# Optimization experiments

Hardware: AMD Instinct MI355X
Metric: run time of the kernel (lower is better)

The kernel has to match this reference:

```python
import jax, jax.numpy as jnp
import numpy as np

EPS = 1e-5
DIM, QK, PDIM = 448, 16, 96

def _bn(y, w, b, rm, rv):
    # inference-mode BatchNorm2d over channel axis 1
    scale = (w / jnp.sqrt(rv + EPS))[None, :, None, None]
    return (y - rm[None, :, None, None]) * scale + b[None, :, None, None]

def setup_inputs() -> dict:
    key = jax.random.key(0)
    ks = jax.random.split(key, 13)
    B, H, W = 64, 32, 32
    return {
        "x": jax.random.normal(ks[0], (B, DIM, H, W), jnp.float32),
        "gn_w": jax.random.uniform(ks[1], (PDIM,), jnp.float32, 0.5, 1.5),
        "gn_b": 0.02 * jax.random.normal(ks[2], (PDIM,), jnp.float32),
        "qkv_w": jax.random.normal(ks[3], (2 * QK + PDIM, PDIM), jnp.float32) * (PDIM ** -0.5),
        "qkv_bn_w": jax.random.uniform(ks[4], (2 * QK + PDIM,), jnp.float32, 0.5, 1.5),
        "qkv_bn_b": 0.02 * jax.random.normal(ks[5], (2 * QK + PDIM,), jnp.float32),
        "qkv_bn_rm": 0.02 * jax.random.normal(ks[6], (2 * QK + PDIM,), jnp.float32),
        "qkv_bn_rv": jax.random.uniform(ks[7], (2 * QK + PDIM,), jnp.float32, 0.5, 1.5),
        "proj_w": jax.random.normal(ks[8], (DIM, DIM), jnp.float32) * (DIM ** -0.5),
        "proj_bn_w": jax.random.uniform(ks[9], (DIM,), jnp.float32, 0.5, 1.5),
        "proj_bn_b": 0.02 * jax.random.normal(ks[10], (DIM,), jnp.float32),
        "proj_bn_rm": 0.02 * jax.random.normal(ks[11], (DIM,), jnp.float32),
        "proj_bn_rv": jax.random.uniform(ks[12], (DIM,), jnp.float32, 0.5, 1.5),
    }

def reference(x, gn_w, gn_b, qkv_w, qkv_bn_w, qkv_bn_b, qkv_bn_rm, qkv_bn_rv,
              proj_w, proj_bn_w, proj_bn_b, proj_bn_rm, proj_bn_rv):
    B, C, H, W = x.shape
    scale = QK ** -0.5
    x1, x2 = x[:, :PDIM], x[:, PDIM:]
    # GroupNorm with num_groups=1: normalize over (C,H,W) per sample
    mu = jnp.mean(x1, axis=(1, 2, 3), keepdims=True)
    var = jnp.var(x1, axis=(1, 2, 3), keepdims=True)
    x1n = (x1 - mu) * jax.lax.rsqrt(var + EPS)
    x1n = x1n * gn_w[None, :, None, None] + gn_b[None, :, None, None]
    # 1x1 conv (no bias) + BN
    qkv = jnp.einsum('bchw,oc->bohw', x1n, qkv_w)
    qkv = _bn(qkv, qkv_bn_w, qkv_bn_b, qkv_bn_rm, qkv_bn_rv)
    q, k, v = qkv[:, :QK], qkv[:, QK:2 * QK], qkv[:, 2 * QK:]
    N = H * W
    q = q.reshape(B, QK, N); k = k.reshape(B, QK, N); v = v.reshape(B, PDIM, N)
    attn = jnp.einsum('bcn,bcm->bnm', q, k) * scale          # [B,N,N]
    attn = jax.nn.softmax(attn, axis=-1)
    x1o = jnp.einsum('bcm,bnm->bcn', v, attn).reshape(B, PDIM, H, W)
    y = jnp.concatenate([x1o, x2], axis=1)
    y = jax.nn.relu(y)
    y = jnp.einsum('bchw,oc->bohw', y, proj_w)
    return _bn(y, proj_bn_w, proj_bn_b, proj_bn_rm, proj_bn_rv)
```

## Files before the change

### kernel.cpp

```cpp
#include <hip/hip_runtime.h>
#include <hip/hip_bf16.h>

#define EPS 1e-5f

constexpr int BB   = 64;
constexpr int CDIM = 448;
constexpr int PD   = 96;
constexpr int QKD  = 16;
constexpr int QO   = 128;
constexpr int NPix = 1024;
constexpr int NCH  = 14;

constexpr size_t WS_MU  = 0;
constexpr size_t WS_RS  = 64;
constexpr size_t WS_QSC = 128;
constexpr size_t WS_QBI = 256;
constexpr size_t WS_PSC = 384;
constexpr size_t WS_PBI = 832;
constexpr size_t WS_WG  = 1280;
constexpr size_t WS_SWG = 13568;
constexpr size_t WS_WB  = 13696;
constexpr size_t WS_WGT = 13824;
constexpr size_t WS_WGH = 26112;
constexpr size_t WS_YB  = 32768;
constexpr size_t WS_W16 = WS_YB + (size_t)BB*NPix*CDIM/2;
constexpr size_t WS_QT  = WS_W16 + (size_t)512*CDIM/2;
constexpr size_t WS_KT  = WS_QT + (size_t)BB*NPix*32/2;
constexpr size_t WS_VB  = WS_KT + (size_t)BB*NPix*32/2;

typedef __attribute__((ext_vector_type(8))) short short8;
typedef __attribute__((ext_vector_type(8))) _Float16 half8;
typedef __attribute__((ext_vector_type(4))) float f32x4;

__device__ __forceinline__ unsigned short f2bf(float v) {
  __hip_bfloat16 h = __float2bfloat16(v);
  return *reinterpret_cast<unsigned short*>(&h);
}
__device__ __forceinline__ unsigned short f2h(float v) {
  _Float16 h = (_Float16)v;
  return *reinterpret_cast<unsigned short*>(&h);
}

typedef const __attribute__((address_space(1))) unsigned int* gp_t;
typedef __attribute__((address_space(3))) unsigned int* lp_t;
__device__ __forceinline__ void gload16(const void* g, void* l) {
  __builtin_amdgcn_global_load_lds((gp_t)g, (lp_t)l, 16, 0, 0);
}

constexpr int XT_BLOCKS = 11264;
constexpr int TAILB     = 209;
__global__ __launch_bounds__(256) void k_setup(
    const float* __restrict__ x,
    const float* __restrict__ gn_w, const float* __restrict__ gn_b,
    const float* __restrict__ qkv_w,
    const float* __restrict__ qbw, const float* __restrict__ qbb,
    const float* __restrict__ qbrm, const float* __restrict__ qbrv,
    const float* __restrict__ pw,
    const float* __restrict__ pbw, const float* __restrict__ pbb,
    const float* __restrict__ pbrm, const float* __restrict__ pbrv,
    float* __restrict__ ws, unsigned short* __restrict__ Wb,
    unsigned short* __restrict__ Ybc) {
  __shared__ float tile[32][65];
  float* red = &tile[0][0];
  int t = threadIdx.x;
  if (blockIdx.x >= TAILB) {
    int idx = blockIdx.x - TAILB;
    int nx = idx & 15, cy = (idx >> 4) % 11, b = idx / 176;
    int c0 = PD + cy * 32;
    int n0 = nx * 64;
#pragma unroll
    for (int i = 0; i < 2; ++i) {
      int k = t + i * 256;
      int c = k >> 4, q = k & 15;
      float4 v = reinterpret_cast<const float4*>(
                     x + ((size_t)b * CDIM + c0 + c) * NPix + n0)[q];
      *reinterpret_cast<float4*>(&tile[c][q * 4]) = v;
    }
    __syncthreads();
    int n = t >> 2, ch = t & 3;
    short8 o;
#pragma unroll
    for (int j = 0; j < 8; ++j)
      o[j] = (short)f2bf(fmaxf(tile[ch * 8 + j][n], 0.f));
    *reinterpret_cast<short8*>(
        &Ybc[(((size_t)b * NCH + 3 + cy) * NPix + n0 + n) * 32 + ch * 8]) = o;
    return;
  }
  int bid = blockIdx.x;
  if (bid < 64) {
    int b = bid;
    const float4* x4 = reinterpret_cast<const float4*>(x + (size_t)b * CDIM * NPix);
    float s = 0.f, ss = 0.f;
#pragma unroll 8
    for (int ii = 0; ii < PD * NPix / 4 / 256; ++ii) {
      float4 v = x4[t + ii * 256];
      s  += v.x + v.y + v.z + v.w;
      ss += v.x * v.x + v.y * v.y + v.z * v.z + v.w * v.w;
    }
#pragma unroll
    for (int o = 32; o > 0; o >>= 1) { s += __shfl_down(s, o); ss += __shfl_down(ss, o); }
    int wid = t >> 6;
    if ((t & 63) == 0) { red[wid] = s; red[4 + wid] = ss; }
    __syncthreads();
    if (t == 0) {
      float S  = red[0] + red[1] + red[2] + red[3];
      float SS = red[4] + red[5] + red[6] + red[7];
      const float inv_n = 1.f / (PD * NPix);
      float mu  = S * inv_n;
      float var = SS * inv_n - mu * mu;
      ws[WS_MU + b] = mu;
      ws[WS_RS + b] = rsqrtf(var + EPS);
    }
  } else if (bid < 96) {
    int o = (bid - 64) * 4 + (t >> 6);
    int lane = t & 63;
    unsigned short* Wgh = reinterpret_cast<unsigned short*>(ws + WS_WGH);
    float sw = 0.f, bb = 0.f;
    for (int c = lane; c < PD; c += 64) {
      float w  = qkv_w[o * PD + c];
      float wg = w * gn_w[c];
      Wgh[(size_t)o * PD + c] = f2h(wg);
      sw += wg;
      bb += w * gn_b[c];
    }
#pragma unroll
    for (int off = 32; off > 0; off >>= 1) {
      sw += __shfl_down(sw, off);
      bb += __shfl_down(bb, off);
    }
    if (lane == 0) {
      ws[WS_SWG + o] = sw;
      ws[WS_WB + o]  = bb;
      float sc = qbw[o] * rsqrtf(qbrv[o] + EPS);
      ws[WS_QSC + o] = sc;
      ws[WS_QBI + o] = qbb[o] - qbrm[o] * sc;
    }
  } else if (bid == 96) {
    for (int o = t; o < CDIM; o += 256) {
      float sc = pbw[o] * rsqrtf(pbrv[o] + EPS);
      ws[WS_PSC + o] = sc;
      ws[WS_PBI + o] = pbb[o] - pbrm[o] * sc;
    }
  } else {
    int idx = (bid - 97) * 256 + t;
    int row = idx / 56, sl = (idx % 56) * 8;
    short8 o = {};
    if (row < CDIM) {
      const float* src = pw + (size_t)row * CDIM + sl;
#pragma unroll
      for (int j = 0; j < 8; ++j) o[j] = (short)f2bf(src[j]);
    }
    *reinterpret_cast<short8*>(&Wb[(size_t)row * CDIM + sl]) = o;
  }
}

__global__ __launch_bounds__(256) void k_qkv2(const float* __restrict__ x,
                                              float* __restrict__ ws,
                                              unsigned short* __restrict__ qt,
                                              unsigned short* __restrict__ kt,
                                              unsigned short* __restrict__ vb) {
  __shared__ __align__(16) char smem[PD * 132 * 4];
  float*          xt = reinterpret_cast<float*>(smem);
  unsigned short* ld = reinterpret_cast<unsigned short*>(smem);

  int lin = blockIdx.x + 8 * blockIdx.y;
  int swz = (lin & 7) * 64 + (lin >> 3);
  int n0  = (swz & 7) * 128;
  int b   = swz >> 3;
  int t   = threadIdx.x;
  int lane = t & 63, w = t >> 6;
  int lo = lane & 15, hi = lane >> 4;

  const float4* xb4 = reinterpret_cast<const float4*>(x + (size_t)b * CDIM * NPix);
#pragma unroll
  for (int i = 0; i < 12; ++i) {
    int idx = t + i * 256;
    int row = idx >> 5, c4 = idx & 31;
    float4 v = xb4[row * (NPix / 4) + (n0 >> 2) + c4];
    *reinterpret_cast<float4*>(&xt[row * 132 + c4 * 4]) = v;
  }
  __syncthreads();

  const unsigned short* Wgh = reinterpret_cast<const unsigned short*>(ws + WS_WGH);
  f32x4 acc[8][2] = {{{}}};
#pragma unroll
  for (int kk = 0; kk < 3; ++kk) {
    half8 bfr[2];
#pragma unroll
    for (int nf = 0; nf < 2; ++nf) {
      int nr = w * 32 + nf * 16 + lo;
      half8 h;
#pragma unroll
      for (int j = 0; j < 8; ++j)
        h[j] = (_Float16)xt[(kk * 32 + hi * 8 + j) * 132 + nr];
      bfr[nf] = h;
    }
#pragma unroll
    for (int of = 0; of < 8; ++of) {
      half8 a = *reinterpret_cast<const half8*>(
          &Wgh[(size_t)(of * 16 + lo) * PD + kk * 32 + hi * 8]);
      acc[of][0] = __builtin_amdgcn_mfma_f32_16x16x32_f16(a, bfr[0], acc[of][0], 0, 0, 0);
      acc[of][1] = __builtin_amdgcn_mfma_f32_16x16x32_f16(a, bfr[1], acc[of][1], 0, 0, 0);
    }
  }
  float mu = ws[WS_MU + b], rs = ws[WS_RS + b];
  __syncthreads();
#pragma unroll
  for (int of = 0; of < 8; ++of) {
#pragma unroll
    for (int r = 0; r < 4; ++r) {
      int o = of * 16 + hi * 4 + r;
      float bias = ws[WS_WB + o] - rs * mu * ws[WS_SWG + o];
      float qs = ws[WS_QSC + o], qb = ws[WS_QBI + o];
      float postm = (o < QKD) ? 0.25f : 1.f;
#pragma unroll
      for (int nf = 0; nf < 2; ++nf) {
        int nl = w * 32 + nf * 16 + lo;
        float v = (qs * (rs * acc[of][nf][r] + bias) + qb) * postm;
        ld[o * 136 + nl] = f2h(v);
      }
    }
  }
  __syncthreads();
#pragma unroll
  for (int i = 0; i < 6; ++i) {
    int idx = t + i * 256;
    int row = idx >> 4, c8 = idx & 15;
    short8 v = *reinterpret_cast<const short8*>(&ld[(32 + row) * 136 + c8 * 8]);
    *reinterpret_cast<short8*>(&vb[((size_t)b * PD + row) * NPix + n0 + c8 * 8]) = v;
  }
#pragma unroll
  for (int i = 0; i < 4; ++i) {
    int idx = t + i * 256;
    int arr = idx >> 9;
    int rem = idx & 511;
    int n = rem >> 2, q4 = rem & 3;
    short8 o = {};
    if (q4 < 2) {
#pragma unroll
      for (int j = 0; j < 8; ++j)
        o[j] = (short)ld[(arr * 16 + q4 * 8 + j) * 136 + n];
    }
    unsigned short* dst = arr ? kt : qt;
    *reinterpret_cast<short8*>(&dst[((size_t)b * NPix + n0 + n) * 32 + q4 * 8]) = o;
  }
}

__global__ __launch_bounds__(512) void k_attn2(
    const unsigned short* __restrict__ qt,
    const unsigned short* __restrict__ kt,
    const unsigned short* __restrict__ vb,
    unsigned short* __restrict__ Ybc) {
  __shared__ __align__(16) unsigned short kt_s[128 * 40];
  __shared__ __align__(16) unsigned short vt_s[96 * 136];
  __shared__ __align__(16) unsigned short P_s[8 * 16 * 136];

  int lin = blockIdx.x + 8 * blockIdx.y;
  int swz = (lin & 7) * 64 + (lin >> 3);
  int n0  = (swz & 7) * 128;
  int b   = swz >> 3;
  int t  = threadIdx.x;
  int lane = t & 63, w = t >> 6;
  int lo = lane & 15, hi = lane >> 4;

  half8 q8 = *reinterpret_cast<const half8*>(
      &qt[((size_t)b * NPix + n0 + w * 16 + lo) * 32 + hi * 8]);

  const unsigned short* ktb = kt + (size_t)b * NPix * 32;
  const unsigned short* vbb = vb + (size_t)b * PD * NPix;

  f32x4 o[6] = {};
  float M = -1e30f, L = 0.f;
  f32x4 zero = {};

  for (int mt = 0; mt < 8; ++mt) {
    int m0 = mt * 128;
    int krow = t >> 2, kc4 = t & 3;
    float4 rk = *reinterpret_cast<const float4*>(&ktb[(size_t)(m0 + krow) * 32 + kc4 * 8]);
    float4 rv[3];
#pragma unroll
    for (int i = 0; i < 3; ++i) {
      int ci = t + 512 * i;
      int row = ci >> 4, c4 = ci & 15;
      rv[i] = *reinterpret_cast<const float4*>(&vbb[(size_t)row * NPix + m0 + c4 * 8]);
    }
    __syncthreads();
    *reinterpret_cast<float4*>(&kt_s[krow * 40 + kc4 * 8]) = rk;
#pragma unroll
    for (int i = 0; i < 3; ++i) {
      int ci = t + 512 * i;
      int row = ci >> 4, c4 = ci & 15;
      *reinterpret_cast<float4*>(&vt_s[row * 136 + c4 * 8]) = rv[i];
    }
    __syncthreads();

    f32x4 s[8];
    __builtin_amdgcn_s_setprio(1);
#pragma unroll
    for (int ss = 0; ss < 8; ++ss) {
      half8 a = *reinterpret_cast<const half8*>(&kt_s[(ss * 16 + lo) * 40 + hi * 8]);
      s[ss] = __builtin_amdgcn_mfma_f32_16x16x32_f16(a, q8, zero, 0, 0, 0);
    }
    __builtin_amdgcn_s_setprio(0);

    float tmax = s[0][0];
#pragma unroll
    for (int ss = 0; ss < 8; ++ss)
#pragma unroll
      for (int r = 0; r < 4; ++r) tmax = fmaxf(tmax, s[ss][r]);
    tmax = fmaxf(tmax, __shfl_xor(tmax, 16));
    tmax = fmaxf(tmax, __shfl_xor(tmax, 32));
    float newM = fmaxf(M, tmax);
    float fac = __expf(M - newM);
    M = newM;
    float psum = 0.f;
    unsigned pbase = (w * 16 + lo) * 136;
#pragma unroll
    for (int ss = 0; ss < 8; ++ss) {
      float p0 = __expf(s[ss][0] - M);
      float p1 = __expf(s[ss][1] - M);
      float p2 = __expf(s[ss][2] - M);
      float p3 = __expf(s[ss][3] - M);
      psum += (p0 + p1) + (p2 + p3);
      unsigned u01 = (unsigned)f2h(p0) | ((unsigned)f2h(p1) << 16);
      unsigned u23 = (unsigned)f2h(p2) | ((unsigned)f2h(p3) << 16);
      *reinterpret_cast<unsigned*>(&P_s[pbase + 16 * ss + 4 * hi])     = u01;
      *reinterpret_cast<unsigned*>(&P_s[pbase + 16 * ss + 4 * hi + 2]) = u23;
    }
    psum += __shfl_xor(psum, 16);
    psum += __shfl_xor(psum, 32);
    L = L * fac + psum;
#pragma unroll
    for (int cf = 0; cf < 6; ++cf)
#pragma unroll
      for (int r = 0; r < 4; ++r) o[cf][r] *= fac;
    asm volatile("s_waitcnt lgkmcnt(0)" ::: "memory");

    __builtin_amdgcn_s_setprio(1);
#pragma unroll
    for (int ks = 0; ks < 4; ++ks) {
      half8 pb = *reinterpret_cast<const half8*>(&P_s[pbase + ks * 32 + hi * 8]);
#pragma unroll
      for (int cf = 0; cf < 6; ++cf) {
        half8 va = *reinterpret_cast<const half8*>(&vt_s[(cf * 16 + lo) * 136 + ks * 32 + hi * 8]);
        o[cf] = __builtin_amdgcn_mfma_f32_16x16x32_f16(va, pb, o[cf], 0, 0, 0);
      }
    }
    __builtin_amdgcn_s_setprio(0);
  }

  float inv = 1.f / L;
  unsigned pbase = (w * 16 + lo) * 136;
#pragma unroll
  for (int cf = 0; cf < 6; ++cf) {
    float v0 = fmaxf(o[cf][0] * inv, 0.f);
    float v1 = fmaxf(o[cf][1] * inv, 0.f);
    float v2 = fmaxf(o[cf][2] * inv, 0.f);
    float v3 = fmaxf(o[cf][3] * inv, 0.f);
    unsigned u01 = (unsigned)f2bf(v0) | ((unsigned)f2bf(v1) << 16);
    unsigned u23 = (unsigned)f2bf(v2) | ((unsigned)f2bf(v3) << 16);
    *reinterpret_cast<unsigned*>(&P_s[pbase + cf * 16 + 4 * hi])     = u01;
    *reinterpret_cast<unsigned*>(&P_s[pbase + cf * 16 + 4 * hi + 2]) = u23;
  }
  asm volatile("s_waitcnt lgkmcnt(0)" ::: "memory");
#pragma unroll
  for (int j = 0; j < 3; ++j) {
    int k = lane + 64 * j;
    int n = k / 12, c8 = k % 12;
    short8 vv = *reinterpret_cast<const short8*>(&P_s[(w * 16 + n) * 136 + c8 * 8]);
    *reinterpret_cast<short8*>(
        &Ybc[(((size_t)b * NCH + (c8 >> 2)) * NPix + n0 + w * 16 + n) * 32
             + (c8 & 3) * 8]) = vv;
  }
}

__global__ __launch_bounds__(256) void k_projmm(
    const unsigned short* __restrict__ Wb,
    const unsigned short* __restrict__ Ybc,
    const float* __restrict__ ws,
    float* __restrict__ out) {
  __shared__ __align__(16) unsigned short At[3][128 * 32];
  __shared__ __align__(16) unsigned short Bt[3][128 * 32];
  int lin = blockIdx.x + 8 * (blockIdx.y + 4 * blockIdx.z);
  int swz = (lin & 7) * 256 + (lin >> 3);
  int m0  = (swz & 3) * 128;
  int n0  = ((swz >> 2) & 7) * 128;
  int b   = swz >> 5;
  int t  = threadIdx.x;
  int lane = t & 63, wid = t >> 6;
  int wm = wid >> 1, wn = wid & 1;

  const unsigned short* Arow = Wb + (size_t)m0 * CDIM;
  const unsigned short* Brow = Ybc + ((size_t)b * NCH * NPix + n0) * 32;

  int chunk0 = wid * 128 + lane;
  int row0 = chunk0 >> 2, sl0 = (chunk0 & 3) ^ ((row0 >> 1) & 3);
  int chunk1 = chunk0 + 64;
  int row1 = chunk1 >> 2, sl1 = (chunk1 & 3) ^ ((row1 >> 1) & 3);

#define STAGE(bufi, s_)                                                        \
  do {                                                                         \
    gload16(Arow + (size_t)row0 * CDIM + (s_) * 32 + sl0 * 8,                  \
            &At[bufi][(wid * 128) * 8]);                                       \
    gload16(Arow + (size_t)row1 * CDIM + (s_) * 32 + sl1 * 8,                  \
            &At[bufi][(wid * 128 + 64) * 8]);                                  \
    gload16(Brow + (size_t)(s_) * NPix * 32 + row0 * 32 + sl0 * 8,             \
            &Bt[bufi][(wid * 128) * 8]);                                       \
    gload16(Brow + (size_t)(s_) * NPix * 32 + row1 * 32 + sl1 * 8,             \
            &Bt[bufi][(wid * 128 + 64) * 8]);                                  \
  } while (0)

  f32x4 acc[4][4] = {{{}}};

  STAGE(0, 0);
  STAGE(1, 1);
  asm volatile("s_waitcnt vmcnt(4) lgkmcnt(0)" ::: "memory");
  __builtin_amdgcn_sched_barrier(0);
  __builtin_amdgcn_s_barrier();

#pragma unroll
  for (int s = 0; s < 14; ++s) {
    if (s + 2 <= 13) STAGE((s + 2) % 3, s + 2);
    short8 af[4], bfr[4];
#pragma unroll
    for (int f = 0; f < 4; ++f) {
      int ar = wm * 64 + f * 16 + (lane & 15);
      int as = (lane >> 4) ^ ((ar >> 1) & 3);
      af[f] = *reinterpret_cast<const short8*>(&At[s % 3][ar * 32 + as * 8]);
      int br = wn * 64 + f * 16 + (lane & 15);
      int bs = (lane >> 4) ^ ((br >> 1) & 3);
      bfr[f] = *reinterpret_cast<const short8*>(&Bt[s % 3][br * 32 + bs * 8]);
    }
#pragma unroll
    for (int i = 0; i < 4; ++i)
#pragma unroll
      for (int j = 0; j < 4; ++j)
        acc[i][j] = __builtin_amdgcn_mfma_f32_16x16x32_bf16(af[i], bfr[j], acc[i][j], 0, 0, 0);
    if (s < 13) {
      if (s <= 11) asm volatile("s_waitcnt vmcnt(4) lgkmcnt(0)" ::: "memory");
      else         asm volatile("s_waitcnt vmcnt(0) lgkmcnt(0)" ::: "memory");
      __builtin_amdgcn_sched_barrier(0);
      __builtin_amdgcn_s_barrier();
    }
  }
#undef STAGE

  int col = lane & 15, rq = lane >> 4;
#pragma unroll
  for (int i = 0; i < 4; ++i) {
    int ob = m0 + wm * 64 + i * 16 + rq * 4;
#pragma unroll
    for (int r = 0; r < 4; ++r) {
      int o = ob + r;
      if (o < CDIM) {
        float ps = ws[WS_PSC + o], pb = ws[WS_PBI + o];
        size_t base = ((size_t)b * CDIM + o) * NPix + n0 + wn * 64 + col;
#pragma unroll
        for (int j = 0; j < 4; ++j)
          out[base + j * 16] = ps * acc[i][j][r] + pb;
      }
    }
  }
}

extern "C" void kernel_launch(void* const* d_in, const int* in_sizes, int n_in,
                              void* d_out, int out_size, void* d_ws, size_t ws_size,
                              hipStream_t stream) {
  const float* x      = (const float*)d_in[0];
  const float* gn_w   = (const float*)d_in[1];
  const float* gn_b   = (const float*)d_in[2];
  const float* qkv_w  = (const float*)d_in[3];
  const float* qbw    = (const float*)d_in[4];
  const float* qbb    = (const float*)d_in[5];
  const float* qbrm   = (const float*)d_in[6];
  const float* qbrv   = (const float*)d_in[7];
  const float* pw     = (const float*)d_in[8];
  const float* pbw    = (const float*)d_in[9];
  const float* pbb    = (const float*)d_in[10];
  const float* pbrm   = (const float*)d_in[11];
  const float* pbrv   = (const float*)d_in[12];
  float* out = (float*)d_out;
  float* ws  = (float*)d_ws;
  unsigned short* Ybc = (unsigned short*)(ws + WS_YB);
  unsigned short* Wb  = (unsigned short*)(ws + WS_W16);
  unsigned short* qt  = (unsigned short*)(ws + WS_QT);
  unsigned short* kt  = (unsigned short*)(ws + WS_KT);
  unsigned short* vb  = (unsigned short*)(ws + WS_VB);

  k_setup<<<TAILB + XT_BLOCKS, 256, 0, stream>>>(
      x, gn_w, gn_b, qkv_w, qbw, qbb, qbrm, qbrv,
      pw, pbw, pbb, pbrm, pbrv, ws, Wb, Ybc);
  k_qkv2<<<dim3(8, BB), 256, 0, stream>>>(x, ws, qt, kt, vb);
  k_attn2<<<dim3(8, BB), 512, 0, stream>>>(qt, kt, vb, Ybc);
  k_projmm<<<dim3(8, 4, BB), 256, 0, stream>>>(Wb, Ybc, ws, out);
}
```

Before: 137.2 us.

## Load projection GEMM fragments directly from global into registers, dropping LDS staging

The projection GEMM no longer stages A and B tiles through triple-buffered shared memory with barriers. Each lane now loads its MFMA fragments straight from global memory into a three-deep register ring, prefetching two steps ahead. This removes LDS traffic, the async-load waits and the block barriers. In exchange every wave re-reads tiles that other waves also need, which doubles global/L2 traffic, and the 24 short8 prefetch registers raise register pressure.

```diff
diff --git a/kernel.cpp b/kernel.cpp
--- a/kernel.cpp
+++ b/kernel.cpp
@@ -379,8 +379,6 @@
     const unsigned short* __restrict__ Ybc,
     const float* __restrict__ ws,
     float* __restrict__ out) {
-  __shared__ __align__(16) unsigned short At[3][128 * 32];
-  __shared__ __align__(16) unsigned short Bt[3][128 * 32];
   int lin = blockIdx.x + 8 * (blockIdx.y + 4 * blockIdx.z);
   int swz = (lin & 7) * 256 + (lin >> 3);
   int m0  = (swz & 3) * 128;
@@ -389,61 +387,41 @@
   int t  = threadIdx.x;
   int lane = t & 63, wid = t >> 6;
   int wm = wid >> 1, wn = wid & 1;
-
-  const unsigned short* Arow = Wb + (size_t)m0 * CDIM;
-  const unsigned short* Brow = Ybc + ((size_t)b * NCH * NPix + n0) * 32;
-
-  int chunk0 = wid * 128 + lane;
-  int row0 = chunk0 >> 2, sl0 = (chunk0 & 3) ^ ((row0 >> 1) & 3);
-  int chunk1 = chunk0 + 64;
-  int row1 = chunk1 >> 2, sl1 = (chunk1 & 3) ^ ((row1 >> 1) & 3);
-
-#define STAGE(bufi, s_)                                                        \
+  int lo = lane & 15, hi = lane >> 4;
+
+  const unsigned short* Abase =
+      Wb + (size_t)(m0 + wm * 64 + lo) * CDIM + hi * 8;
+  const unsigned short* Bbase =
+      Ybc + ((size_t)b * NCH * NPix + n0 + wn * 64 + lo) * 32 + hi * 8;
+
+  short8 af[3][4], bf[3][4];
+  f32x4 acc[4][4] = {{{}}};
+
+#define LOAD_STEP(slot, s_)                                                    \
   do {                                                                         \
-    gload16(Arow + (size_t)row0 * CDIM + (s_) * 32 + sl0 * 8,                  \
-            &At[bufi][(wid * 128) * 8]);                                       \
-    gload16(Arow + (size_t)row1 * CDIM + (s_) * 32 + sl1 * 8,                  \
-            &At[bufi][(wid * 128 + 64) * 8]);                                  \
-    gload16(Brow + (size_t)(s_) * NPix * 32 + row0 * 32 + sl0 * 8,             \
-            &Bt[bufi][(wid * 128) * 8]);                                       \
-    gload16(Brow + (size_t)(s_) * NPix * 32 + row1 * 32 + sl1 * 8,             \
-            &Bt[bufi][(wid * 128 + 64) * 8]);                                  \
+    _Pragma("unroll")                                                          \
+    for (int f = 0; f < 4; ++f) {                                              \
+      af[slot][f] = *reinterpret_cast<const short8*>(                          \
+          Abase + (size_t)f * 16 * CDIM + (s_) * 32);                          \
+      bf[slot][f] = *reinterpret_cast<const short8*>(                          \
+          Bbase + (size_t)(s_) * NPix * 32 + f * 16 * 32);                     \
+    }                                                                          \
   } while (0)
 
-  f32x4 acc[4][4] = {{{}}};
-
-  STAGE(0, 0);
-  STAGE(1, 1);
-  asm volatile("s_waitcnt vmcnt(4) lgkmcnt(0)" ::: "memory");
-  __builtin_amdgcn_sched_barrier(0);
-  __builtin_amdgcn_s_barrier();
+  LOAD_STEP(0, 0);
+  LOAD_STEP(1, 1);
 
 #pragma unroll
   for (int s = 0; s < 14; ++s) {
-    if (s + 2 <= 13) STAGE((s + 2) % 3, s + 2);
-    short8 af[4], bfr[4];
-#pragma unroll
-    for (int f = 0; f < 4; ++f) {
-      int ar = wm * 64 + f * 16 + (lane & 15);
-      int as = (lane >> 4) ^ ((ar >> 1) & 3);
-      af[f] = *reinterpret_cast<const short8*>(&At[s % 3][ar * 32 + as * 8]);
-      int br = wn * 64 + f * 16 + (lane & 15);
-      int bs = (lane >> 4) ^ ((br >> 1) & 3);
-      bfr[f] = *reinterpret_cast<const short8*>(&Bt[s % 3][br * 32 + bs * 8]);
-    }
+    if (s + 2 < 14) LOAD_STEP((s + 2) % 3, s + 2);
 #pragma unroll
     for (int i = 0; i < 4; ++i)
 #pragma unroll
       for (int j = 0; j < 4; ++j)
-        acc[i][j] = __builtin_amdgcn_mfma_f32_16x16x32_bf16(af[i], bfr[j], acc[i][j], 0, 0, 0);
-    if (s < 13) {
-      if (s <= 11) asm volatile("s_waitcnt vmcnt(4) lgkmcnt(0)" ::: "memory");
-      else         asm volatile("s_waitcnt vmcnt(0) lgkmcnt(0)" ::: "memory");
-      __builtin_amdgcn_sched_barrier(0);
-      __builtin_amdgcn_s_barrier();
-    }
-  }
-#undef STAGE
+        acc[i][j] = __builtin_amdgcn_mfma_f32_16x16x32_bf16(
+            af[s % 3][i], bf[s % 3][j], acc[i][j], 0, 0, 0);
+  }
+#undef LOAD_STEP
 
   int col = lane & 15, rq = lane >> 4;
 #pragma unroll
```

After: 181.1 us. +32.0%, slower.
